# Optimization experiments

Hardware: AMD Instinct MI355X
Metric: run time of the kernel (lower is better)

## Reference

```python
import jax, jax.numpy as jnp
import numpy as np

NUM_EMBEDDINGS = 512
EMBEDDING_DIM = 64


def setup_inputs() -> dict:
    key = jax.random.key(0)
    k_in, k_emb = jax.random.split(key)
    inputs = jax.random.normal(k_in, (8, 64, 16, 32, 32), dtype=jnp.float32)
    # matches torch uniform_(-1/K, 1/K) init
    lim = 1.0 / NUM_EMBEDDINGS
    embedding = jax.random.uniform(
        k_emb, (NUM_EMBEDDINGS, EMBEDDING_DIM), dtype=jnp.float32,
        minval=-lim, maxval=lim)
    return {"inputs": inputs, "embedding": embedding}


def reference(inputs, embedding):
    # inputs: (B, C=D, T, H, W); embedding: (K, D)
    x = jnp.transpose(inputs, (0, 2, 3, 4, 1))  # (B, T, H, W, D)
    in_shape = x.shape
    flat = x.reshape(-1, EMBEDDING_DIM)  # (N, D)
    distances = (
        jnp.sum(flat * flat, axis=1, keepdims=True)
        + jnp.sum(embedding * embedding, axis=1)
        - 2.0 * jnp.matmul(flat, embedding.T)
    )  # (N, K)
    # NOTE: original applies softmax to raw (positive) distances, faithfully kept
    weights = jax.nn.softmax(distances, axis=1)
    out = jnp.matmul(weights, embedding).reshape(in_shape)  # (B,T,H,W,D)
    return jnp.transpose(out, (0, 4, 1, 2, 3))  # (B, D, T, H, W)
```

## Files before the change

### kernel.cpp

```cpp
#include <hip/hip_runtime.h>
#include <hip/hip_bf16.h>

typedef __attribute__((ext_vector_type(8))) short short8;
typedef __attribute__((ext_vector_type(4))) short short4v;
typedef __attribute__((ext_vector_type(8))) _Float16 half8;
typedef __attribute__((ext_vector_type(2))) __fp16 fp16x2;
typedef __attribute__((ext_vector_type(4))) float f32x4;

#define SPW 16384
#define XST 72
#define RW  67
#define LOG2E 1.4426950408889634f

__device__ __forceinline__ float exp2_hw(float f) {
  return __builtin_amdgcn_exp2f(f);
}

__device__ __forceinline__ short bf16s(float f) {
  union { __hip_bfloat16 h; short s; } u;
  u.h = __float2bfloat16(f);
  return u.s;
}

__global__ void prep_all(const float* __restrict__ emb, short8* __restrict__ a1b,
                         half8* __restrict__ eb3, float* __restrict__ norms) {
  const int f = blockIdx.x * 256 + threadIdx.x;
  if (f < 4096) {
    const int s = f & 1;
    const int lane = (f >> 1) & 63;
    const int kt = f >> 7;
    const int row = kt * 16 + (lane & 15);
    const int col0 = s * 32 + (lane >> 4) * 8;
    short8 v;
    #pragma unroll
    for (int i = 0; i < 8; ++i)
      v[i] = bf16s(-2.0f * LOG2E * emb[row * 64 + col0 + i]);
    a1b[f] = v;
  } else if (f < 8192) {
    const int e = f - 4096;
    const int m2 = e & 3;
    const int lane = (e >> 2) & 63;
    const int pr = e >> 8;
    const int g = lane >> 4;
    const int d = m2 * 16 + (lane & 15);
    half8 v;
    #pragma unroll
    for (int i = 0; i < 8; ++i) {
      const int k = (i < 4) ? (pr * 32 + 4 * g + i) : (pr * 32 + 16 + 4 * g + (i - 4));
      v[i] = (_Float16)emb[k * 64 + d];
    }
    eb3[e] = v;
  } else if (f < 8704) {
    const int k = f - 8192;
    float acc = 0.f;
    #pragma unroll
    for (int d = 0; d < 64; ++d) { float e = emb[k * 64 + d]; acc += e * e; }
    norms[k] = acc * LOG2E;
  }
}

struct Frags {
  short8 aA0, aA1, aB0, aB1;
  half8 e0, e1, e2, e3;
  float4 nvA, nvB;
};

__device__ __forceinline__ void ldfrag(Frags& f, const short8* __restrict__ a1b,
                                       const half8* __restrict__ eb3,
                                       const float* __restrict__ norms,
                                       int pr, int lane, int g) {
  const int ktA = pr * 2;
  f.nvA = *reinterpret_cast<const float4*>(&norms[ktA * 16 + g * 4]);
  f.nvB = *reinterpret_cast<const float4*>(&norms[ktA * 16 + 16 + g * 4]);
  const short8* ap = &a1b[(ktA * 64 + lane) * 2];
  f.aA0 = ap[0];
  f.aA1 = ap[1];
  f.aB0 = ap[128];
  f.aB1 = ap[129];
  const half8* ep = &eb3[(pr * 64 + lane) * 4];
  f.e0 = ep[0];
  f.e1 = ep[1];
  f.e2 = ep[2];
  f.e3 = ep[3];
}

__device__ __forceinline__ half8 make_pa(float p0, float p1, float p2, float p3,
                                         float p4, float p5, float p6, float p7) {
  const unsigned a = __builtin_bit_cast(unsigned, __builtin_amdgcn_cvt_pkrtz(p0, p1));
  const unsigned b = __builtin_bit_cast(unsigned, __builtin_amdgcn_cvt_pkrtz(p2, p3));
  const unsigned c = __builtin_bit_cast(unsigned, __builtin_amdgcn_cvt_pkrtz(p4, p5));
  const unsigned d = __builtin_bit_cast(unsigned, __builtin_amdgcn_cvt_pkrtz(p6, p7));
  const uint4 u = {a, b, c, d};
  return __builtin_bit_cast(half8, u);
}

__device__ __forceinline__ void compute_unit(const Frags& f, const short8 bx[4][2],
                                             f32x4 pacc[4][4], f32x4 dacc[4],
                                             const half8 ones) {
  #pragma unroll
  for (int j = 0; j < 4; ++j) {
    f32x4 zA = {f.nvA.x, f.nvA.y, f.nvA.z, f.nvA.w};
    zA = __builtin_amdgcn_mfma_f32_16x16x32_bf16(f.aA0, bx[j][0], zA, 0, 0, 0);
    zA = __builtin_amdgcn_mfma_f32_16x16x32_bf16(f.aA1, bx[j][1], zA, 0, 0, 0);
    f32x4 zB = {f.nvB.x, f.nvB.y, f.nvB.z, f.nvB.w};
    zB = __builtin_amdgcn_mfma_f32_16x16x32_bf16(f.aB0, bx[j][0], zB, 0, 0, 0);
    zB = __builtin_amdgcn_mfma_f32_16x16x32_bf16(f.aB1, bx[j][1], zB, 0, 0, 0);
    const float p0 = exp2_hw(zA[0]);
    const float p1 = exp2_hw(zA[1]);
    const float p2 = exp2_hw(zA[2]);
    const float p3 = exp2_hw(zA[3]);
    const float p4 = exp2_hw(zB[0]);
    const float p5 = exp2_hw(zB[1]);
    const float p6 = exp2_hw(zB[2]);
    const float p7 = exp2_hw(zB[3]);
    const half8 pa = make_pa(p0, p1, p2, p3, p4, p5, p6, p7);
    pacc[j][0] = __builtin_amdgcn_mfma_f32_16x16x32_f16(pa, f.e0, pacc[j][0], 0, 0, 0);
    pacc[j][1] = __builtin_amdgcn_mfma_f32_16x16x32_f16(pa, f.e1, pacc[j][1], 0, 0, 0);
    pacc[j][2] = __builtin_amdgcn_mfma_f32_16x16x32_f16(pa, f.e2, pacc[j][2], 0, 0, 0);
    pacc[j][3] = __builtin_amdgcn_mfma_f32_16x16x32_f16(pa, f.e3, pacc[j][3], 0, 0, 0);
    dacc[j] = __builtin_amdgcn_mfma_f32_16x16x32_f16(pa, ones, dacc[j], 0, 0, 0);
  }
}

__global__ __launch_bounds__(256, 2) void vq_main(
    const float* __restrict__ x, const short8* __restrict__ a1b,
    const half8* __restrict__ eb3, const float* __restrict__ norms,
    float* __restrict__ out) {
  __shared__ __align__(16) char lds_raw[35840];
  short* Xl   = reinterpret_cast<short*>(lds_raw);
  float* Rf   = reinterpret_cast<float*>(lds_raw);
  float* denl = reinterpret_cast<float*>(lds_raw + 34304);
  float* rden = reinterpret_cast<float*>(lds_raw + 35328);

  const int t = threadIdx.x;
  const int lane = t & 63;
  const int w = t >> 6;
  const int cg = w & 1;
  const int kg = w >> 1;
  const int l15 = lane & 15;
  const int g = lane >> 4;

  const int tile = blockIdx.x * 128;
  const int b = tile >> 14;
  const int off = tile & 16383;
  const float* xb = x + (size_t)b * (64 * SPW) + off;
  float* ob = out + (size_t)b * (64 * SPW) + off;

  {
    const int n0 = 4 * (t & 15);
    const int d0 = 4 * (t >> 4);
    #pragma unroll
    for (int h = 0; h < 2; ++h) {
      const int nb = h * 64 + n0;
      const float4 r0 = *reinterpret_cast<const float4*>(xb + (size_t)(d0 + 0) * SPW + nb);
      const float4 r1 = *reinterpret_cast<const float4*>(xb + (size_t)(d0 + 1) * SPW + nb);
      const float4 r2 = *reinterpret_cast<const float4*>(xb + (size_t)(d0 + 2) * SPW + nb);
      const float4 r3 = *reinterpret_cast<const float4*>(xb + (size_t)(d0 + 3) * SPW + nb);
      const short4v c0 = {bf16s(r0.x), bf16s(r1.x), bf16s(r2.x), bf16s(r3.x)};
      const short4v c1 = {bf16s(r0.y), bf16s(r1.y), bf16s(r2.y), bf16s(r3.y)};
      const short4v c2 = {bf16s(r0.z), bf16s(r1.z), bf16s(r2.z), bf16s(r3.z)};
      const short4v c3 = {bf16s(r0.w), bf16s(r1.w), bf16s(r2.w), bf16s(r3.w)};
      *reinterpret_cast<short4v*>(&Xl[(nb + 0) * XST + d0]) = c0;
      *reinterpret_cast<short4v*>(&Xl[(nb + 1) * XST + d0]) = c1;
      *reinterpret_cast<short4v*>(&Xl[(nb + 2) * XST + d0]) = c2;
      *reinterpret_cast<short4v*>(&Xl[(nb + 3) * XST + d0]) = c3;
    }
  }
  __syncthreads();

  short8 bx[4][2];
  #pragma unroll
  for (int j = 0; j < 4; ++j) {
    const int base = (cg * 64 + j * 16 + l15) * XST + g * 8;
    bx[j][0] = *reinterpret_cast<const short8*>(&Xl[base]);
    bx[j][1] = *reinterpret_cast<const short8*>(&Xl[base + 32]);
  }
  __syncthreads();

  f32x4 pacc[4][4];
  #pragma unroll
  for (int j = 0; j < 4; ++j)
    #pragma unroll
    for (int m2 = 0; m2 < 4; ++m2) pacc[j][m2] = f32x4{0.f, 0.f, 0.f, 0.f};
  f32x4 dacc[4];
  #pragma unroll
  for (int j = 0; j < 4; ++j) dacc[j] = f32x4{0.f, 0.f, 0.f, 0.f};
  const half8 ones = {(_Float16)1.f, (_Float16)1.f, (_Float16)1.f, (_Float16)1.f,
                      (_Float16)1.f, (_Float16)1.f, (_Float16)1.f, (_Float16)1.f};

  const int prb = kg * 8;
  Frags fA, fB;
  ldfrag(fA, a1b, eb3, norms, prb + 0, lane, g);
  #pragma unroll
  for (int p2 = 0; p2 < 4; ++p2) {
    ldfrag(fB, a1b, eb3, norms, prb + 2 * p2 + 1, lane, g);
    compute_unit(fA, bx, pacc, dacc, ones);
    if (p2 < 3) ldfrag(fA, a1b, eb3, norms, prb + 2 * p2 + 2, lane, g);
    compute_unit(fB, bx, pacc, dacc, ones);
  }

  if (l15 == 0) {
    #pragma unroll
    for (int j = 0; j < 4; ++j)
      #pragma unroll
      for (int r = 0; r < 4; ++r)
        denl[kg * 128 + cg * 64 + j * 16 + 4 * g + r] = dacc[j][r];
  }

  if (kg == 0) {
    #pragma unroll
    for (int j = 0; j < 4; ++j)
      #pragma unroll
      for (int m2 = 0; m2 < 4; ++m2)
        #pragma unroll
        for (int r = 0; r < 4; ++r)
          Rf[(cg * 64 + j * 16 + 4 * g + r) * RW + m2 * 16 + l15] = pacc[j][m2][r];
  }
  __syncthreads();

  if (kg == 1) {
    #pragma unroll
    for (int j = 0; j < 4; ++j)
      #pragma unroll
      for (int m2 = 0; m2 < 4; ++m2)
        #pragma unroll
        for (int r = 0; r < 4; ++r)
          Rf[(cg * 64 + j * 16 + 4 * g + r) * RW + m2 * 16 + l15] += pacc[j][m2][r];
  } else {
    rden[t & 127] = 1.0f / (denl[t & 127] + denl[128 + (t & 127)]);
  }
  __syncthreads();

  const int nq = t & 31;
  const int n = 4 * nq;
  const int dh = t >> 5;
  #pragma unroll
  for (int it = 0; it < 8; ++it) {
    const int d = it * 8 + dh;
    const float4 o = {Rf[(n + 0) * RW + d] * rden[n + 0],
                      Rf[(n + 1) * RW + d] * rden[n + 1],
                      Rf[(n + 2) * RW + d] * rden[n + 2],
                      Rf[(n + 3) * RW + d] * rden[n + 3]};
    *reinterpret_cast<float4*>(&ob[(size_t)d * SPW + n]) = o;
  }
}

extern "C" void kernel_launch(void* const* d_in, const int* in_sizes, int n_in,
                              void* d_out, int out_size, void* d_ws, size_t ws_size,
                              hipStream_t stream) {
  (void)in_sizes; (void)n_in; (void)out_size; (void)ws_size;
  const float* x   = (const float*)d_in[0];
  const float* emb = (const float*)d_in[1];
  float* out = (float*)d_out;

  char* ws = (char*)d_ws;
  short8* a1b  = (short8*)ws;
  half8*  eb3  = (half8*)(ws + 65536);
  float*  norms = (float*)(ws + 131072);

  prep_all<<<34, 256, 0, stream>>>(emb, a1b, eb3, norms);
  vq_main<<<1024, 256, 0, stream>>>(x, a1b, eb3, norms, out);
}
```

Baseline: 38.03 us.

## Shrink tile to 32 points with four-way codebook split across waves

```diff
diff --git a/kernel.cpp b/kernel.cpp
--- a/kernel.cpp
+++ b/kernel.cpp
@@ -9,7 +9,7 @@
 
 #define SPW 16384
 #define XST 72
-#define RW  67
+#define RW  66
 #define LOG2E 1.4426950408889634f
 
 __device__ __forceinline__ float exp2_hw(float f) {
@@ -94,11 +94,11 @@
   return __builtin_bit_cast(half8, u);
 }
 
-__device__ __forceinline__ void compute_unit(const Frags& f, const short8 bx[4][2],
-                                             f32x4 pacc[4][4], f32x4 dacc[4],
+__device__ __forceinline__ void compute_unit(const Frags& f, const short8 bx[2][2],
+                                             f32x4 pacc[2][4], f32x4 dacc[2],
                                              const half8 ones) {
   #pragma unroll
-  for (int j = 0; j < 4; ++j) {
+  for (int j = 0; j < 2; ++j) {
     f32x4 zA = {f.nvA.x, f.nvA.y, f.nvA.z, f.nvA.w};
     zA = __builtin_amdgcn_mfma_f32_16x16x32_bf16(f.aA0, bx[j][0], zA, 0, 0, 0);
     zA = __builtin_amdgcn_mfma_f32_16x16x32_bf16(f.aA1, bx[j][1], zA, 0, 0, 0);
@@ -122,126 +122,111 @@
   }
 }
 
-__global__ __launch_bounds__(256, 2) void vq_main(
+__global__ __launch_bounds__(256, 3) void vq_main(
     const float* __restrict__ x, const short8* __restrict__ a1b,
     const half8* __restrict__ eb3, const float* __restrict__ norms,
     float* __restrict__ out) {
-  __shared__ __align__(16) char lds_raw[35840];
+  __shared__ __align__(16) char lds_raw[34432];
   short* Xl   = reinterpret_cast<short*>(lds_raw);
   float* Rf   = reinterpret_cast<float*>(lds_raw);
-  float* denl = reinterpret_cast<float*>(lds_raw + 34304);
-  float* rden = reinterpret_cast<float*>(lds_raw + 35328);
+  float* denl = reinterpret_cast<float*>(lds_raw + 33792);
 
   const int t = threadIdx.x;
   const int lane = t & 63;
-  const int w = t >> 6;
-  const int cg = w & 1;
-  const int kg = w >> 1;
+  const int kg = t >> 6;
   const int l15 = lane & 15;
   const int g = lane >> 4;
 
-  const int tile = blockIdx.x * 128;
+  const int tile = blockIdx.x * 32;
   const int b = tile >> 14;
   const int off = tile & 16383;
   const float* xb = x + (size_t)b * (64 * SPW) + off;
   float* ob = out + (size_t)b * (64 * SPW) + off;
 
-  {
-    const int n0 = 4 * (t & 15);
-    const int d0 = 4 * (t >> 4);
-    #pragma unroll
-    for (int h = 0; h < 2; ++h) {
-      const int nb = h * 64 + n0;
-      const float4 r0 = *reinterpret_cast<const float4*>(xb + (size_t)(d0 + 0) * SPW + nb);
-      const float4 r1 = *reinterpret_cast<const float4*>(xb + (size_t)(d0 + 1) * SPW + nb);
-      const float4 r2 = *reinterpret_cast<const float4*>(xb + (size_t)(d0 + 2) * SPW + nb);
-      const float4 r3 = *reinterpret_cast<const float4*>(xb + (size_t)(d0 + 3) * SPW + nb);
-      const short4v c0 = {bf16s(r0.x), bf16s(r1.x), bf16s(r2.x), bf16s(r3.x)};
-      const short4v c1 = {bf16s(r0.y), bf16s(r1.y), bf16s(r2.y), bf16s(r3.y)};
-      const short4v c2 = {bf16s(r0.z), bf16s(r1.z), bf16s(r2.z), bf16s(r3.z)};
-      const short4v c3 = {bf16s(r0.w), bf16s(r1.w), bf16s(r2.w), bf16s(r3.w)};
-      *reinterpret_cast<short4v*>(&Xl[(nb + 0) * XST + d0]) = c0;
-      *reinterpret_cast<short4v*>(&Xl[(nb + 1) * XST + d0]) = c1;
-      *reinterpret_cast<short4v*>(&Xl[(nb + 2) * XST + d0]) = c2;
-      *reinterpret_cast<short4v*>(&Xl[(nb + 3) * XST + d0]) = c3;
-    }
+  if (t < 128) {
+    const int n0 = 4 * (t & 7);
+    const int d0 = 4 * (t >> 3);
+    const float4 r0 = *reinterpret_cast<const float4*>(xb + (size_t)(d0 + 0) * SPW + n0);
+    const float4 r1 = *reinterpret_cast<const float4*>(xb + (size_t)(d0 + 1) * SPW + n0);
+    const float4 r2 = *reinterpret_cast<const float4*>(xb + (size_t)(d0 + 2) * SPW + n0);
+    const float4 r3 = *reinterpret_cast<const float4*>(xb + (size_t)(d0 + 3) * SPW + n0);
+    const short4v c0 = {bf16s(r0.x), bf16s(r1.x), bf16s(r2.x), bf16s(r3.x)};
+    const short4v c1 = {bf16s(r0.y), bf16s(r1.y), bf16s(r2.y), bf16s(r3.y)};
+    const short4v c2 = {bf16s(r0.z), bf16s(r1.z), bf16s(r2.z), bf16s(r3.z)};
+    const short4v c3 = {bf16s(r0.w), bf16s(r1.w), bf16s(r2.w), bf16s(r3.w)};
+    *reinterpret_cast<short4v*>(&Xl[(n0 + 0) * XST + d0]) = c0;
+    *reinterpret_cast<short4v*>(&Xl[(n0 + 1) * XST + d0]) = c1;
+    *reinterpret_cast<short4v*>(&Xl[(n0 + 2) * XST + d0]) = c2;
+    *reinterpret_cast<short4v*>(&Xl[(n0 + 3) * XST + d0]) = c3;
   }
   __syncthreads();
 
-  short8 bx[4][2];
-  #pragma unroll
-  for (int j = 0; j < 4; ++j) {
-    const int base = (cg * 64 + j * 16 + l15) * XST + g * 8;
+  short8 bx[2][2];
+  #pragma unroll
+  for (int j = 0; j < 2; ++j) {
+    const int base = (j * 16 + l15) * XST + g * 8;
     bx[j][0] = *reinterpret_cast<const short8*>(&Xl[base]);
     bx[j][1] = *reinterpret_cast<const short8*>(&Xl[base + 32]);
   }
   __syncthreads();
 
-  f32x4 pacc[4][4];
-  #pragma unroll
-  for (int j = 0; j < 4; ++j)
+  f32x4 pacc[2][4];
+  #pragma unroll
+  for (int j = 0; j < 2; ++j)
     #pragma unroll
     for (int m2 = 0; m2 < 4; ++m2) pacc[j][m2] = f32x4{0.f, 0.f, 0.f, 0.f};
-  f32x4 dacc[4];
-  #pragma unroll
-  for (int j = 0; j < 4; ++j) dacc[j] = f32x4{0.f, 0.f, 0.f, 0.f};
+  f32x4 dacc[2] = {f32x4{0.f, 0.f, 0.f, 0.f}, f32x4{0.f, 0.f, 0.f, 0.f}};
   const half8 ones = {(_Float16)1.f, (_Float16)1.f, (_Float16)1.f, (_Float16)1.f,
                       (_Float16)1.f, (_Float16)1.f, (_Float16)1.f, (_Float16)1.f};
 
-  const int prb = kg * 8;
+  const int prb = kg * 4;
   Frags fA, fB;
   ldfrag(fA, a1b, eb3, norms, prb + 0, lane, g);
-  #pragma unroll
-  for (int p2 = 0; p2 < 4; ++p2) {
-    ldfrag(fB, a1b, eb3, norms, prb + 2 * p2 + 1, lane, g);
-    compute_unit(fA, bx, pacc, dacc, ones);
-    if (p2 < 3) ldfrag(fA, a1b, eb3, norms, prb + 2 * p2 + 2, lane, g);
-    compute_unit(fB, bx, pacc, dacc, ones);
-  }
+  ldfrag(fB, a1b, eb3, norms, prb + 1, lane, g);
+  compute_unit(fA, bx, pacc, dacc, ones);
+  ldfrag(fA, a1b, eb3, norms, prb + 2, lane, g);
+  compute_unit(fB, bx, pacc, dacc, ones);
+  ldfrag(fB, a1b, eb3, norms, prb + 3, lane, g);
+  compute_unit(fA, bx, pacc, dacc, ones);
+  compute_unit(fB, bx, pacc, dacc, ones);
 
   if (l15 == 0) {
     #pragma unroll
-    for (int j = 0; j < 4; ++j)
+    for (int j = 0; j < 2; ++j)
       #pragma unroll
       for (int r = 0; r < 4; ++r)
-        denl[kg * 128 + cg * 64 + j * 16 + 4 * g + r] = dacc[j][r];
-  }
-
-  if (kg == 0) {
-    #pragma unroll
-    for (int j = 0; j < 4; ++j)
+        denl[kg * 32 + j * 16 + 4 * g + r] = dacc[j][r];
+  }
+
+  #pragma unroll
+  for (int j = 0; j < 2; ++j)
+    #pragma unroll
+    for (int m2 = 0; m2 < 4; ++m2)
       #pragma unroll
-      for (int m2 = 0; m2 < 4; ++m2)
-        #pragma unroll
-        for (int r = 0; r < 4; ++r)
-          Rf[(cg * 64 + j * 16 + 4 * g + r) * RW + m2 * 16 + l15] = pacc[j][m2][r];
-  }
+      for (int r = 0; r < 4; ++r)
+        Rf[(kg * 32 + j * 16 + 4 * g + r) * RW + m2 * 16 + l15] = pacc[j][m2][r];
   __syncthreads();
 
-  if (kg == 1) {
-    #pragma unroll
-    for (int j = 0; j < 4; ++j)
-      #pragma unroll
-      for (int m2 = 0; m2 < 4; ++m2)
-        #pragma unroll
-        for (int r = 0; r < 4; ++r)
-          Rf[(cg * 64 + j * 16 + 4 * g + r) * RW + m2 * 16 + l15] += pacc[j][m2][r];
-  } else {
-    rden[t & 127] = 1.0f / (denl[t & 127] + denl[128 + (t & 127)]);
-  }
-  __syncthreads();
-
-  const int nq = t & 31;
-  const int n = 4 * nq;
-  const int dh = t >> 5;
-  #pragma unroll
-  for (int it = 0; it < 8; ++it) {
-    const int d = it * 8 + dh;
-    const float4 o = {Rf[(n + 0) * RW + d] * rden[n + 0],
-                      Rf[(n + 1) * RW + d] * rden[n + 1],
-                      Rf[(n + 2) * RW + d] * rden[n + 2],
-                      Rf[(n + 3) * RW + d] * rden[n + 3]};
-    *reinterpret_cast<float4*>(&ob[(size_t)d * SPW + n]) = o;
+  const int n4 = 4 * (t & 7);
+  const int dbase = t >> 3;
+  f32x4 rd;
+  #pragma unroll
+  for (int i = 0; i < 4; ++i) {
+    const int n = n4 + i;
+    rd[i] = 1.0f / ((denl[n] + denl[32 + n]) + (denl[64 + n] + denl[96 + n]));
+  }
+  #pragma unroll
+  for (int it = 0; it < 2; ++it) {
+    const int d = it * 32 + dbase;
+    float4 o;
+    #pragma unroll
+    for (int i = 0; i < 4; ++i) {
+      const int n = n4 + i;
+      const float s = (Rf[n * RW + d] + Rf[(32 + n) * RW + d])
+                    + (Rf[(64 + n) * RW + d] + Rf[(96 + n) * RW + d]);
+      reinterpret_cast<float*>(&o)[i] = s * rd[i];
+    }
+    *reinterpret_cast<float4*>(&ob[(size_t)d * SPW + n4]) = o;
   }
 }
 
@@ -259,5 +244,5 @@
   float*  norms = (float*)(ws + 131072);
 
   prep_all<<<34, 256, 0, stream>>>(emb, a1b, eb3, norms);
-  vq_main<<<1024, 256, 0, stream>>>(x, a1b, eb3, norms, out);
-}
+  vq_main<<<4096, 256, 0, stream>>>(x, a1b, eb3, norms, out);
+}
```

Measured after the change: 46.62 us. 22.6% more time.

## Process two tiles per block with register prefetch of next input tile

Applied to the files above, without the earlier changes.

```diff
diff --git a/kernel.cpp b/kernel.cpp
--- a/kernel.cpp
+++ b/kernel.cpp
@@ -4,7 +4,6 @@
 typedef __attribute__((ext_vector_type(8))) short short8;
 typedef __attribute__((ext_vector_type(4))) short short4v;
 typedef __attribute__((ext_vector_type(8))) _Float16 half8;
-typedef __attribute__((ext_vector_type(2))) __fp16 fp16x2;
 typedef __attribute__((ext_vector_type(4))) float f32x4;
 
 #define SPW 16384
@@ -122,6 +121,39 @@
   }
 }
 
+__device__ __forceinline__ void ldx(float4 xr[8], const float* __restrict__ xb, int t) {
+  const int n0 = 4 * (t & 15);
+  const int d0 = 4 * (t >> 4);
+  #pragma unroll
+  for (int h = 0; h < 2; ++h) {
+    const int nb = h * 64 + n0;
+    #pragma unroll
+    for (int i = 0; i < 4; ++i)
+      xr[h * 4 + i] = *reinterpret_cast<const float4*>(xb + (size_t)(d0 + i) * SPW + nb);
+  }
+}
+
+__device__ __forceinline__ void stx(const float4 xr[8], short* Xl, int t) {
+  const int n0 = 4 * (t & 15);
+  const int d0 = 4 * (t >> 4);
+  #pragma unroll
+  for (int h = 0; h < 2; ++h) {
+    const int nb = h * 64 + n0;
+    const float4 r0 = xr[h * 4 + 0];
+    const float4 r1 = xr[h * 4 + 1];
+    const float4 r2 = xr[h * 4 + 2];
+    const float4 r3 = xr[h * 4 + 3];
+    const short4v c0 = {bf16s(r0.x), bf16s(r1.x), bf16s(r2.x), bf16s(r3.x)};
+    const short4v c1 = {bf16s(r0.y), bf16s(r1.y), bf16s(r2.y), bf16s(r3.y)};
+    const short4v c2 = {bf16s(r0.z), bf16s(r1.z), bf16s(r2.z), bf16s(r3.z)};
+    const short4v c3 = {bf16s(r0.w), bf16s(r1.w), bf16s(r2.w), bf16s(r3.w)};
+    *reinterpret_cast<short4v*>(&Xl[(nb + 0) * XST + d0]) = c0;
+    *reinterpret_cast<short4v*>(&Xl[(nb + 1) * XST + d0]) = c1;
+    *reinterpret_cast<short4v*>(&Xl[(nb + 2) * XST + d0]) = c2;
+    *reinterpret_cast<short4v*>(&Xl[(nb + 3) * XST + d0]) = c3;
+  }
+}
+
 __global__ __launch_bounds__(256, 2) void vq_main(
     const float* __restrict__ x, const short8* __restrict__ a1b,
     const half8* __restrict__ eb3, const float* __restrict__ norms,
@@ -139,109 +171,107 @@
   const int kg = w >> 1;
   const int l15 = lane & 15;
   const int g = lane >> 4;
-
-  const int tile = blockIdx.x * 128;
-  const int b = tile >> 14;
-  const int off = tile & 16383;
-  const float* xb = x + (size_t)b * (64 * SPW) + off;
-  float* ob = out + (size_t)b * (64 * SPW) + off;
-
-  {
-    const int n0 = 4 * (t & 15);
-    const int d0 = 4 * (t >> 4);
-    #pragma unroll
-    for (int h = 0; h < 2; ++h) {
-      const int nb = h * 64 + n0;
-      const float4 r0 = *reinterpret_cast<const float4*>(xb + (size_t)(d0 + 0) * SPW + nb);
-      const float4 r1 = *reinterpret_cast<const float4*>(xb + (size_t)(d0 + 1) * SPW + nb);
-      const float4 r2 = *reinterpret_cast<const float4*>(xb + (size_t)(d0 + 2) * SPW + nb);
-      const float4 r3 = *reinterpret_cast<const float4*>(xb + (size_t)(d0 + 3) * SPW + nb);
-      const short4v c0 = {bf16s(r0.x), bf16s(r1.x), bf16s(r2.x), bf16s(r3.x)};
-      const short4v c1 = {bf16s(r0.y), bf16s(r1.y), bf16s(r2.y), bf16s(r3.y)};
-      const short4v c2 = {bf16s(r0.z), bf16s(r1.z), bf16s(r2.z), bf16s(r3.z)};
-      const short4v c3 = {bf16s(r0.w), bf16s(r1.w), bf16s(r2.w), bf16s(r3.w)};
-      *reinterpret_cast<short4v*>(&Xl[(nb + 0) * XST + d0]) = c0;
-      *reinterpret_cast<short4v*>(&Xl[(nb + 1) * XST + d0]) = c1;
-      *reinterpret_cast<short4v*>(&Xl[(nb + 2) * XST + d0]) = c2;
-      *reinterpret_cast<short4v*>(&Xl[(nb + 3) * XST + d0]) = c3;
-    }
-  }
-  __syncthreads();
-
-  short8 bx[4][2];
-  #pragma unroll
-  for (int j = 0; j < 4; ++j) {
-    const int base = (cg * 64 + j * 16 + l15) * XST + g * 8;
-    bx[j][0] = *reinterpret_cast<const short8*>(&Xl[base]);
-    bx[j][1] = *reinterpret_cast<const short8*>(&Xl[base + 32]);
-  }
-  __syncthreads();
-
-  f32x4 pacc[4][4];
-  #pragma unroll
-  for (int j = 0; j < 4; ++j)
-    #pragma unroll
-    for (int m2 = 0; m2 < 4; ++m2) pacc[j][m2] = f32x4{0.f, 0.f, 0.f, 0.f};
-  f32x4 dacc[4];
-  #pragma unroll
-  for (int j = 0; j < 4; ++j) dacc[j] = f32x4{0.f, 0.f, 0.f, 0.f};
+  const int prb = kg * 8;
+
   const half8 ones = {(_Float16)1.f, (_Float16)1.f, (_Float16)1.f, (_Float16)1.f,
                       (_Float16)1.f, (_Float16)1.f, (_Float16)1.f, (_Float16)1.f};
 
-  const int prb = kg * 8;
-  Frags fA, fB;
-  ldfrag(fA, a1b, eb3, norms, prb + 0, lane, g);
-  #pragma unroll
-  for (int p2 = 0; p2 < 4; ++p2) {
-    ldfrag(fB, a1b, eb3, norms, prb + 2 * p2 + 1, lane, g);
-    compute_unit(fA, bx, pacc, dacc, ones);
-    if (p2 < 3) ldfrag(fA, a1b, eb3, norms, prb + 2 * p2 + 2, lane, g);
-    compute_unit(fB, bx, pacc, dacc, ones);
-  }
-
-  if (l15 == 0) {
+  float4 xr[8], xrn[8];
+  {
+    const int tile0 = blockIdx.x * 128;
+    ldx(xr, x + (size_t)(tile0 >> 14) * (64 * SPW) + (tile0 & 16383), t);
+  }
+
+  #pragma unroll 1
+  for (int tt = 0; tt < 2; ++tt) {
+    const int tile = (blockIdx.x + tt * 512) * 128;
+    float* ob = out + (size_t)(tile >> 14) * (64 * SPW) + (tile & 16383);
+
+    stx(xr, Xl, t);
+    __syncthreads();
+
+    short8 bx[4][2];
+    #pragma unroll
+    for (int j = 0; j < 4; ++j) {
+      const int base = (cg * 64 + j * 16 + l15) * XST + g * 8;
+      bx[j][0] = *reinterpret_cast<const short8*>(&Xl[base]);
+      bx[j][1] = *reinterpret_cast<const short8*>(&Xl[base + 32]);
+    }
+    __syncthreads();
+
+    if (tt == 0) {
+      const int tile1 = (blockIdx.x + 512) * 128;
+      ldx(xrn, x + (size_t)(tile1 >> 14) * (64 * SPW) + (tile1 & 16383), t);
+      __builtin_amdgcn_sched_barrier(0);
+    }
+
+    f32x4 pacc[4][4];
     #pragma unroll
     for (int j = 0; j < 4; ++j)
       #pragma unroll
-      for (int r = 0; r < 4; ++r)
-        denl[kg * 128 + cg * 64 + j * 16 + 4 * g + r] = dacc[j][r];
-  }
-
-  if (kg == 0) {
-    #pragma unroll
-    for (int j = 0; j < 4; ++j)
-      #pragma unroll
-      for (int m2 = 0; m2 < 4; ++m2)
+      for (int m2 = 0; m2 < 4; ++m2) pacc[j][m2] = f32x4{0.f, 0.f, 0.f, 0.f};
+    f32x4 dacc[4];
+    #pragma unroll
+    for (int j = 0; j < 4; ++j) dacc[j] = f32x4{0.f, 0.f, 0.f, 0.f};
+
+    Frags fA, fB;
+    ldfrag(fA, a1b, eb3, norms, prb + 0, lane, g);
+    #pragma unroll
+    for (int p2 = 0; p2 < 4; ++p2) {
+      ldfrag(fB, a1b, eb3, norms, prb + 2 * p2 + 1, lane, g);
+      compute_unit(fA, bx, pacc, dacc, ones);
+      if (p2 < 3) ldfrag(fA, a1b, eb3, norms, prb + 2 * p2 + 2, lane, g);
+      compute_unit(fB, bx, pacc, dacc, ones);
+    }
+
+    if (l15 == 0) {
+      #pragma unroll
+      for (int j = 0; j < 4; ++j)
         #pragma unroll
         for (int r = 0; r < 4; ++r)
-          Rf[(cg * 64 + j * 16 + 4 * g + r) * RW + m2 * 16 + l15] = pacc[j][m2][r];
-  }
-  __syncthreads();
-
-  if (kg == 1) {
-    #pragma unroll
-    for (int j = 0; j < 4; ++j)
-      #pragma unroll
-      for (int m2 = 0; m2 < 4; ++m2)
+          denl[kg * 128 + cg * 64 + j * 16 + 4 * g + r] = dacc[j][r];
+    }
+
+    if (kg == 0) {
+      #pragma unroll
+      for (int j = 0; j < 4; ++j)
         #pragma unroll
-        for (int r = 0; r < 4; ++r)
-          Rf[(cg * 64 + j * 16 + 4 * g + r) * RW + m2 * 16 + l15] += pacc[j][m2][r];
-  } else {
-    rden[t & 127] = 1.0f / (denl[t & 127] + denl[128 + (t & 127)]);
-  }
-  __syncthreads();
-
-  const int nq = t & 31;
-  const int n = 4 * nq;
-  const int dh = t >> 5;
-  #pragma unroll
-  for (int it = 0; it < 8; ++it) {
-    const int d = it * 8 + dh;
-    const float4 o = {Rf[(n + 0) * RW + d] * rden[n + 0],
-                      Rf[(n + 1) * RW + d] * rden[n + 1],
-                      Rf[(n + 2) * RW + d] * rden[n + 2],
-                      Rf[(n + 3) * RW + d] * rden[n + 3]};
-    *reinterpret_cast<float4*>(&ob[(size_t)d * SPW + n]) = o;
+        for (int m2 = 0; m2 < 4; ++m2)
+          #pragma unroll
+          for (int r = 0; r < 4; ++r)
+            Rf[(cg * 64 + j * 16 + 4 * g + r) * RW + m2 * 16 + l15] = pacc[j][m2][r];
+    }
+    __syncthreads();
+
+    if (kg == 1) {
+      #pragma unroll
+      for (int j = 0; j < 4; ++j)
+        #pragma unroll
+        for (int m2 = 0; m2 < 4; ++m2)
+          #pragma unroll
+          for (int r = 0; r < 4; ++r)
+            Rf[(cg * 64 + j * 16 + 4 * g + r) * RW + m2 * 16 + l15] += pacc[j][m2][r];
+    } else {
+      rden[t & 127] = 1.0f / (denl[t & 127] + denl[128 + (t & 127)]);
+    }
+    __syncthreads();
+
+    const int nq = t & 31;
+    const int n = 4 * nq;
+    const int dh = t >> 5;
+    #pragma unroll
+    for (int it = 0; it < 8; ++it) {
+      const int d = it * 8 + dh;
+      const float4 o = {Rf[(n + 0) * RW + d] * rden[n + 0],
+                        Rf[(n + 1) * RW + d] * rden[n + 1],
+                        Rf[(n + 2) * RW + d] * rden[n + 2],
+                        Rf[(n + 3) * RW + d] * rden[n + 3]};
+      *reinterpret_cast<float4*>(&ob[(size_t)d * SPW + n]) = o;
+    }
+    __syncthreads();
+
+    #pragma unroll
+    for (int i = 0; i < 8; ++i) xr[i] = xrn[i];
   }
 }
 
@@ -259,5 +289,5 @@
   float*  norms = (float*)(ws + 131072);
 
   prep_all<<<34, 256, 0, stream>>>(emb, a1b, eb3, norms);
-  vq_main<<<1024, 256, 0, stream>>>(x, a1b, eb3, norms, out);
-}
+  vq_main<<<512, 256, 0, stream>>>(x, a1b, eb3, norms, out);
+}
```

New measurement: 123.0 us. 3.24x slower.
